# Kernel tuning notes

Measured on AMD Instinct MI355X. Metric: run time of the kernel, lower is better.

## Reference

```python
import jax, jax.numpy as jnp
from jax import lax
import numpy as np

B = 8192
NUM_CTX = 300; NUM_STN = 300; NUM_GPE = 20; NUM_GPI = 2; NUM_OUT = 20
FF_DIM = 20; FF_STEPS = 20; STN_ITERS = 50
ETA_GPE = 1.0; ETA_STN = 1.0 / 3.0; ETA_GPI = 0.1
A1 = 1.0; A2 = 1.0; THETAD1 = 0.0; THETAD2 = 0.0
UNITS = (64, 128, 64)

_SPECS = [("vf0", UNITS[0], NUM_CTX), ("vf1", UNITS[1], UNITS[0]), ("vf2", UNITS[2], UNITS[1]), ("vf3", 1, UNITS[2]),
          ("jd1", FF_DIM, NUM_CTX), ("jd2", FF_DIM, NUM_CTX), ("kd1", FF_DIM, NUM_CTX), ("kd2", FF_DIM, NUM_CTX),
          ("sg", NUM_GPE, NUM_STN), ("gs", NUM_STN, NUM_GPE), ("glat", NUM_GPE, NUM_GPE), ("slat", NUM_STN, NUM_STN),
          ("d1gpi", NUM_GPI, FF_DIM), ("stngpi", NUM_GPI, NUM_STN),
          ("ih", 4 * NUM_OUT, NUM_GPI), ("hh", 4 * NUM_OUT, NUM_OUT)]


def _lin_init(k, out_d, in_d):
    kw, kb = jax.random.split(k)
    bound = 1.0 / np.sqrt(in_d)
    w = jax.random.uniform(kw, (out_d, in_d), minval=-bound, maxval=bound, dtype=jnp.float32)
    b = jax.random.uniform(kb, (out_d,), minval=-bound, maxval=bound, dtype=jnp.float32)
    return w, b


def setup_inputs() -> dict:
    key = jax.random.key(0)
    ks = iter(jax.random.split(key, 40))
    inp = {}
    inp["stimulus"] = jax.random.normal(next(ks), (B, NUM_CTX), dtype=jnp.float32)
    inp["deltavf"] = jax.random.normal(next(ks), (B, 1), dtype=jnp.float32)
    inp["hx0"] = jax.random.uniform(next(ks), (B, NUM_OUT), dtype=jnp.float32)
    inp["cx0"] = jax.random.uniform(next(ks), (B, NUM_OUT), dtype=jnp.float32)
    for name, o, i in _SPECS:
        w, b = _lin_init(next(ks), o, i)
        inp["w_" + name] = w
        inp["b_" + name] = b
    return inp


def _lin(x, w, b):
    return x @ w.T + b


def _lstm_cell(x, h, c, w_ih, b_ih, w_hh, b_hh):
    gates = _lin(x, w_ih, b_ih) + _lin(h, w_hh, b_hh)
    i, f, g, o = jnp.split(gates, 4, axis=-1)  # torch LSTMCell gate order
    c_new = jax.nn.sigmoid(f) * c + jax.nn.sigmoid(i) * jnp.tanh(g)
    h_new = jax.nn.sigmoid(o) * jnp.tanh(c_new)
    return h_new, c_new


def reference(stimulus, deltavf, hx0, cx0,
              w_vf0, b_vf0, w_vf1, b_vf1, w_vf2, b_vf2, w_vf3, b_vf3,
              w_jd1, b_jd1, w_jd2, b_jd2, w_kd1, b_kd1, w_kd2, b_kd2,
              w_sg, b_sg, w_gs, b_gs, w_glat, b_glat, w_slat, b_slat,
              w_d1gpi, b_d1gpi, w_stngpi, b_stngpi,
              w_ih, b_ih, w_hh, b_hh):
    bsz = stimulus.shape[0]
    # value function head
    h = jax.nn.relu(_lin(stimulus, w_vf0, b_vf0))
    h = jax.nn.relu(_lin(h, w_vf1, b_vf1))
    h = jax.nn.relu(_lin(h, w_vf2, b_vf2))
    vt = jnp.tanh(_lin(h, w_vf3, b_vf3))  # [B, 1]

    lamd1 = jax.nn.sigmoid(A1 * (deltavf - THETAD1))  # [B, 1]
    lamd2 = jax.nn.sigmoid(A2 * (deltavf - THETAD2))  # [B, 1]

    # loop-invariant striatal drives (computed every iter in torch, same value)
    J_D1 = _lin(stimulus, w_jd1, b_jd1)
    J_D2 = _lin(stimulus, w_jd2, b_jd2)
    K_D1 = _lin(stimulus, w_kd1, b_kd1)
    K_D2 = _lin(stimulus, w_kd2, b_kd2)

    def ff_step(carry, _):
        v1, v2 = carry
        v1 = jax.nn.sigmoid(lamd1 * (J_D1 * (1.0 - v1) + (1.0 - K_D1) * v1))
        v2 = jax.nn.sigmoid(lamd2 * (J_D2 * (1.0 - v2) + (1.0 - K_D2) * v2))
        return (v1, v2), None

    z_ff = jnp.zeros((bsz, FF_DIM), dtype=stimulus.dtype)
    (V_D1, V_D2), _ = lax.scan(ff_step, (z_ff, z_ff), None, length=FF_STEPS)

    V_GPi_DP = _lin(V_D1, w_d1gpi, b_d1gpi)  # [B, num_gpi]

    def stn_step(carry, _):
        xgpe, xstn, vstn, vgpi, hx, cx = carry
        xgpe = xgpe + ETA_GPE * (-xgpe + _lin(vstn, w_sg, b_sg) + _lin(xgpe, w_glat, b_glat) - V_D2)
        xstn = xstn + ETA_STN * (-xstn + _lin(xgpe, w_gs, b_gs) + _lin(vstn, w_slat, b_slat))
        vstn = jnp.tanh(lamd2 * xstn)
        V_GPi_IP = lamd2 * _lin(vstn, w_stngpi, b_stngpi)
        vgpi = vgpi + ETA_GPI * (-vgpi - V_GPi_DP + 2.0 * V_GPi_IP)
        hx, cx = _lstm_cell(-vgpi, hx, cx, w_ih, b_ih, w_hh, b_hh)
        return (xgpe, xstn, vstn, vgpi, hx, cx), None

    carry0 = (jnp.zeros((bsz, NUM_GPE), dtype=stimulus.dtype),
              jnp.zeros((bsz, NUM_STN), dtype=stimulus.dtype),
              jnp.zeros((bsz, NUM_STN), dtype=stimulus.dtype),  # tanh(lamd2*0) = 0
              jnp.zeros((bsz, NUM_GPI), dtype=stimulus.dtype),
              hx0, cx0)
    carry, _ = lax.scan(stn_step, carry0, None, length=STN_ITERS)
    hx = carry[4]
    return hx, vt
```

## Files before the change

### kernel.cpp

```cpp
#include <hip/hip_runtime.h>


typedef _Float16 f16_t;
typedef _Float16 f16x8 __attribute__((ext_vector_type(8)));
typedef _Float16 f16x4 __attribute__((ext_vector_type(4)));
typedef float floatx4 __attribute__((ext_vector_type(4)));
typedef float floatx2 __attribute__((ext_vector_type(2)));

#define BTOT 8192
#define BM   32
#define NTHR 512
#define NBLK 256
#define VSTR 328
#define XST  32

struct Params {
  const float *stimulus, *deltavf, *hx0, *cx0;
  const float *w_vf0, *b_vf0, *w_vf1, *b_vf1, *w_vf2, *b_vf2, *w_vf3, *b_vf3;
  const float *w_jd1, *b_jd1, *w_jd2, *b_jd2, *w_kd1, *b_kd1, *w_kd2, *b_kd2;
  const float *w_sg, *b_sg, *w_gs, *b_gs, *w_glat, *b_glat, *w_slat, *b_slat;
  const float *w_d1gpi, *b_d1gpi, *w_stngpi, *b_stngpi;
  const float *w_ih, *b_ih, *w_hh, *b_hh;
  float* out;
};

struct __align__(16) Smem {
  f16_t vstn[BM * VSTR];
  f16_t xgpe[2][BM * XST];
  f16_t hxf[BM * XST];
  f16_t wB2[21 * 512];
  f16_t wsp[10 * 512];
  f16_t whh[5 * 512];
  union { float h1f[BM * 128]; float scr[3200]; float gates[BM * 80]; } u;
  float h0f[BM * 64];
  float V_D2f[BM * 20];
  float lstmc[20][12];
  float bsumS[304];
  float bsg[20];
  float DPs[BM * 2], vgpis[BM * 2], lamS[BM];
};

__device__ __forceinline__ float rcp_f(float x) { return __builtin_amdgcn_rcpf(x); }
__device__ __forceinline__ float sigm_fast(float x) { return rcp_f(1.f + __expf(-x)); }
__device__ __forceinline__ float tanh_fast(float x) { return 1.f - 2.f * rcp_f(1.f + __expf(2.f * x)); }

__device__ __forceinline__ f16x8 ldfrag(const float* row, int k0, int kmax, bool valid) {
  float4 z = make_float4(0.f, 0.f, 0.f, 0.f);
  int nv = valid ? (kmax - k0) : 0;
  float4 f0 = (nv >= 4) ? *(const float4*)(row + k0) : z;
  float4 f1 = (nv >= 8) ? *(const float4*)(row + k0 + 4) : z;
  f16x8 r;
  r[0] = (f16_t)f0.x; r[1] = (f16_t)f0.y; r[2] = (f16_t)f0.z; r[3] = (f16_t)f0.w;
  r[4] = (f16_t)f1.x; r[5] = (f16_t)f1.y; r[6] = (f16_t)f1.z; r[7] = (f16_t)f1.w;
  return r;
}

__global__ __launch_bounds__(NTHR, 2) void bg_main(Params P) {
  __shared__ Smem S;
  const int tid  = threadIdx.x;
  const int lane = tid & 63;
  const int wv   = tid >> 6;
  const int q    = lane >> 4;
  const int cl   = lane & 15;
  const int row0 = blockIdx.x * BM;
  const floatx4 zf = {0.f, 0.f, 0.f, 0.f};

  if (tid < BM) S.lamS[tid] = sigm_fast(P.deltavf[row0 + tid]);
  for (int i = tid; i < BM * 2; i += NTHR) S.vgpis[i] = 0.f;
  for (int i = tid; i < 2 * BM * XST; i += NTHR) ((f16_t*)S.xgpe)[i] = (f16_t)0.f;
  for (int i = tid; i < BM * XST; i += NTHR) {
    int m = i >> 5, j = i & 31;
    S.hxf[i] = (j < 20) ? (f16_t)P.hx0[row0 * 20 + m * 20 + j] : (f16_t)0.f;
  }
  for (int i = tid; i < BM * VSTR; i += NTHR) S.vstn[i] = (f16_t)0.f;
  for (int i = tid; i < 21 * 512; i += NTHR) {
    int t = i >> 9, l = (i >> 3) & 63, jj = i & 7;
    int c2 = l & 15, k = ((l >> 4) << 3) + jj;
    float v = 0.f;
    if (t < 19) { int n = t * 16 + c2; if (n < 300 && k < 20) v = P.w_gs[n * 20 + k]; }
    else        { int g = (t - 19) * 16 + c2; if (g < 20 && k < 20) v = P.w_glat[g * 20 + k]; }
    S.wB2[i] = (f16_t)v;
  }
  for (int i = tid; i < 10 * 512; i += NTHR) {
    int c = i >> 9, l = (i >> 3) & 63, jj = i & 7;
    int p = l & 15, k = c * 32 + ((l >> 4) << 3) + jj;
    float v = (p < 2 && k < 300) ? P.w_stngpi[p * 300 + k] : 0.f;
    S.wsp[i] = (f16_t)v;
  }
  for (int i = tid; i < 5 * 512; i += NTHR) {
    int t = i >> 9, l = (i >> 3) & 63, jj = i & 7;
    int c2 = l & 15, k = ((l >> 4) << 3) + jj;
    int orig = (c2 & 3) * 20 + 4 * t + (c2 >> 2);
    S.whh[i] = (f16_t)((k < 20) ? P.w_hh[orig * 20 + k] : 0.f);
  }
  for (int i = tid; i < 240; i += NTHR) {
    int j = i / 12, c = i - j * 12;
    float v;
    if (c < 4)      v = P.b_ih[c * 20 + j] + P.b_hh[c * 20 + j];
    else if (c < 8) v = P.w_ih[((c - 4) * 20 + j) * 2 + 0];
    else            v = P.w_ih[((c - 8) * 20 + j) * 2 + 1];
    S.lstmc[j][c] = v;
  }
  for (int i = tid; i < 304; i += NTHR) S.bsumS[i] = (i < 300) ? (P.b_slat[i] + P.b_gs[i]) : 0.f;
  for (int i = tid; i < 20; i += NTHR)  S.bsg[i] = P.b_sg[i] + P.b_glat[i];

  {
    int o = tid & 63, mb = (tid >> 6) * 4;
    const float4* wr = (const float4*)(P.w_vf0 + o * 300);
    float bias = P.b_vf0[o], a[4];
#pragma unroll
    for (int u = 0; u < 4; ++u) a[u] = bias;
    for (int kq = 0; kq < 75; ++kq) {
      float4 w = wr[kq];
#pragma unroll
      for (int u = 0; u < 4; ++u) {
        float4 v = *(const float4*)(P.stimulus + (size_t)(row0 + mb + u) * 300 + kq * 4);
        a[u] = fmaf(v.x, w.x, a[u]); a[u] = fmaf(v.y, w.y, a[u]);
        a[u] = fmaf(v.z, w.z, a[u]); a[u] = fmaf(v.w, w.w, a[u]);
      }
    }
#pragma unroll
    for (int u = 0; u < 4; ++u) S.h0f[(mb + u) * 64 + o] = fmaxf(a[u], 0.f);
  }
  __syncthreads();
  {
    int o = tid & 127, mb = (tid >> 7) * 8;
    const float* wr = P.w_vf1 + o * 64;
    float bias = P.b_vf1[o], a[8];
#pragma unroll
    for (int u = 0; u < 8; ++u) a[u] = bias;
    for (int k = 0; k < 64; ++k) {
      float w = wr[k];
#pragma unroll
      for (int u = 0; u < 8; ++u) a[u] = fmaf(S.h0f[(mb + u) * 64 + k], w, a[u]);
    }
#pragma unroll
    for (int u = 0; u < 8; ++u) S.u.h1f[(mb + u) * 128 + o] = fmaxf(a[u], 0.f);
  }
  __syncthreads();
  {
    int o = tid & 63, mb = (tid >> 6) * 4;
    const float* wr = P.w_vf2 + o * 128;
    float bias = P.b_vf2[o], a[4];
#pragma unroll
    for (int u = 0; u < 4; ++u) a[u] = bias;
    for (int k = 0; k < 128; ++k) {
      float w = wr[k];
#pragma unroll
      for (int u = 0; u < 4; ++u) a[u] = fmaf(S.u.h1f[(mb + u) * 128 + k], w, a[u]);
    }
#pragma unroll
    for (int u = 0; u < 4; ++u) S.h0f[(mb + u) * 64 + o] = fmaxf(a[u], 0.f);
  }
  __syncthreads();
  {
    int oid = tid & 127, mb = (tid >> 7) * 8;
    if (oid < 80) {
      int which = oid / 20, o = oid - which * 20;
      const float *wp, *bp;
      if (which == 0)      { wp = P.w_jd1; bp = P.b_jd1; }
      else if (which == 1) { wp = P.w_jd2; bp = P.b_jd2; }
      else if (which == 2) { wp = P.w_kd1; bp = P.b_kd1; }
      else                 { wp = P.w_kd2; bp = P.b_kd2; }
      float bias = bp[o], a[8];
#pragma unroll
      for (int u = 0; u < 8; ++u) a[u] = bias;
      for (int kq = 0; kq < 75; ++kq) {
        float4 w = *(const float4*)(wp + o * 300 + kq * 4);
#pragma unroll
        for (int u = 0; u < 8; ++u) {
          float4 v = *(const float4*)(P.stimulus + (size_t)(row0 + mb + u) * 300 + kq * 4);
          a[u] = fmaf(v.x, w.x, a[u]); a[u] = fmaf(v.y, w.y, a[u]);
          a[u] = fmaf(v.z, w.z, a[u]); a[u] = fmaf(v.w, w.w, a[u]);
        }
      }
#pragma unroll
      for (int u = 0; u < 8; ++u) S.u.scr[which * 640 + (mb + u) * 20 + o] = a[u];
    }
    if (tid < BM) {
      float a = P.b_vf3[0];
      for (int k = 0; k < 64; ++k) a = fmaf(S.h0f[tid * 64 + k], P.w_vf3[k], a);
      P.out[(size_t)BTOT * 20 + row0 + tid] = tanh_fast(a);
    }
  }
  __syncthreads();
  for (int i = tid; i < BM * 20; i += NTHR) {
    int m = i / 20;
    float j1 = S.u.scr[i],        j2 = S.u.scr[640 + i];
    float k1 = S.u.scr[1280 + i], k2 = S.u.scr[1920 + i];
    float L = S.lamS[m], v1 = 0.f, v2 = 0.f;
    for (int s = 0; s < 20; ++s) {
      v1 = sigm_fast(L * (j1 * (1.f - v1) + (1.f - k1) * v1));
      v2 = sigm_fast(L * (j2 * (1.f - v2) + (1.f - k2) * v2));
    }
    S.u.scr[2560 + i] = v1;
    S.V_D2f[i] = v2;
  }
  __syncthreads();
  if (tid < BM * 2) {
    int m = tid >> 1, p2 = tid & 1;
    float a = P.b_d1gpi[p2];
    for (int o = 0; o < 20; ++o) a = fmaf(S.u.scr[2560 + m * 20 + o], P.w_d1gpi[p2 * 20 + o], a);
    S.DPs[tid] = a;
  }
  __syncthreads();

  f16x8 Ws[3][10];
#pragma unroll
  for (int j = 0; j < 3; ++j) {
    int t = wv + 8 * j;
    if (t < 19) {
      int n = t * 16 + cl;
#pragma unroll
      for (int c = 0; c < 10; ++c)
        Ws[j][c] = ldfrag(P.w_slat + (size_t)(n < 300 ? n : 0) * 300, c * 32 + q * 8, 300, n < 300);
    } else if (t < 21) {
      int g = (t - 19) * 16 + cl;
#pragma unroll
      for (int c = 0; c < 10; ++c)
        Ws[j][c] = ldfrag(P.w_sg + (size_t)(g < 20 ? g : 0) * 300, c * 32 + q * 8, 300, g < 20);
    } else {
      f16x8 z;
#pragma unroll
      for (int e = 0; e < 8; ++e) z[e] = (f16_t)0.f;
#pragma unroll
      for (int c = 0; c < 10; ++c) Ws[j][c] = z;
    }
  }
  const float lam0 = S.lamS[cl], lam1 = S.lamS[cl + 16];
  const float bstn0 = P.b_stngpi[0], bstn1 = P.b_stngpi[1];
  const int e0 = tid,        m0 = e0 / 20, j0 = e0 - m0 * 20;
  const int e1 = tid + NTHR, m1 = e1 / 20, j1 = e1 - m1 * 20;
  const bool hase1 = (tid < BM * 20 - NTHR);
  float cxr0 = P.cx0[row0 * 20 + e0], hxr0 = P.hx0[row0 * 20 + e0];
  float cxr1 = hase1 ? P.cx0[row0 * 20 + e1] : 0.f;
  float hxr1 = hase1 ? P.hx0[row0 * 20 + e1] : 0.f;
  const bool isSgW = (wv == 3 || wv == 4);

  floatx4 acc[3][2];
#pragma unroll
  for (int j = 0; j < 3; ++j) { acc[j][0] = zf; acc[j][1] = zf; }

  for (int g = 0; g <= 50; ++g) {
    const bool run = (g < 50), ran = (g > 0);
    const int po = g & 1, pn = po ^ 1;

    if (run) {
      if (isSgW) { acc[2][0] = zf; acc[2][1] = zf; }
      __builtin_amdgcn_s_setprio(1);
#pragma unroll
      for (int c = 0; c < 10; ++c) {
        f16x8 b0 = *(const f16x8*)&S.vstn[cl * VSTR + c * 32 + q * 8];
        f16x8 b1 = *(const f16x8*)&S.vstn[(16 + cl) * VSTR + c * 32 + q * 8];
#pragma unroll
        for (int j = 0; j < 3; ++j) {
          if (wv + 8 * j < 21) {
            acc[j][0] = __builtin_amdgcn_mfma_f32_16x16x32_f16(Ws[j][c], b0, acc[j][0], 0, 0, 0);
            acc[j][1] = __builtin_amdgcn_mfma_f32_16x16x32_f16(Ws[j][c], b1, acc[j][1], 0, 0, 0);
          }
        }
      }
      __builtin_amdgcn_s_setprio(0);
      if (isSgW) {
        f16x8 Wg = *(const f16x8*)&S.wB2[(wv + 16) * 512 + lane * 8];
        f16x8 g0 = *(const f16x8*)&S.xgpe[po][cl * XST + q * 8];
        f16x8 g1 = *(const f16x8*)&S.xgpe[po][(16 + cl) * XST + q * 8];
        acc[2][0] = __builtin_amdgcn_mfma_f32_16x16x32_f16(Wg, g0, acc[2][0], 0, 0, 0);
        acc[2][1] = __builtin_amdgcn_mfma_f32_16x16x32_f16(Wg, g1, acc[2][1], 0, 0, 0);
        int g0i = (wv - 3) * 16 + q * 4;
        if (g0i < 20) {
          floatx4 bg4 = *(const floatx4*)&S.bsg[g0i];
#pragma unroll
          for (int mf = 0; mf < 2; ++mf) {
            int batch = cl + 16 * mf;
            floatx4 vd4 = *(const floatx4*)&S.V_D2f[batch * 20 + g0i];
            f16x4 pk;
#pragma unroll
            for (int r = 0; r < 4; ++r) pk[r] = (f16_t)(acc[2][mf][r] + bg4[r] - vd4[r]);
            *(f16x4*)&S.xgpe[pn][batch * XST + g0i] = pk;
          }
        }
      }
    }
    if (ran && wv == 5) {
      floatx4 ip0 = zf, ip1 = zf;
#pragma unroll
      for (int c = 0; c < 10; ++c) {
        f16x8 Wp = *(const f16x8*)&S.wsp[c * 512 + lane * 8];
        f16x8 b0 = *(const f16x8*)&S.vstn[cl * VSTR + c * 32 + q * 8];
        f16x8 b1 = *(const f16x8*)&S.vstn[(16 + cl) * VSTR + c * 32 + q * 8];
        ip0 = __builtin_amdgcn_mfma_f32_16x16x32_f16(Wp, b0, ip0, 0, 0, 0);
        ip1 = __builtin_amdgcn_mfma_f32_16x16x32_f16(Wp, b1, ip1, 0, 0, 0);
      }
      if (q == 0) {
#pragma unroll
        for (int mf = 0; mf < 2; ++mf) {
          int batch = cl + 16 * mf;
          float lm = mf ? lam1 : lam0;
          floatx2 vg = *(const floatx2*)&S.vgpis[batch * 2];
          floatx2 dp = *(const floatx2*)&S.DPs[batch * 2];
          float ipa = lm * ((mf ? ip1[0] : ip0[0]) + bstn0);
          float ipb = lm * ((mf ? ip1[1] : ip0[1]) + bstn1);
          vg[0] = vg[0] + 0.1f * (-vg[0] - dp[0] + 2.f * ipa);
          vg[1] = vg[1] + 0.1f * (-vg[1] - dp[1] + 2.f * ipb);
          *(floatx2*)&S.vgpis[batch * 2] = vg;
        }
      }
    }
    if (ran && (wv == 6 || wv == 7)) {
      int tb = (wv == 6) ? 0 : 3;
      int tc = (wv == 6) ? 3 : 2;
      for (int tt = 0; tt < tc; ++tt) {
        int t = tb + tt;
        f16x8 Wh = *(const f16x8*)&S.whh[t * 512 + lane * 8];
        f16x8 h0 = *(const f16x8*)&S.hxf[cl * XST + q * 8];
        f16x8 h1 = *(const f16x8*)&S.hxf[(16 + cl) * XST + q * 8];
        floatx4 gA = __builtin_amdgcn_mfma_f32_16x16x32_f16(Wh, h0, zf, 0, 0, 0);
        floatx4 gB = __builtin_amdgcn_mfma_f32_16x16x32_f16(Wh, h1, zf, 0, 0, 0);
        int gb = t * 16 + q * 4;
        *(floatx4*)&S.u.gates[cl * 80 + gb] = gA;
        *(floatx4*)&S.u.gates[(cl + 16) * 80 + gb] = gB;
      }
    }
    __syncthreads();

    if (run) {
      f16x8 x0 = *(const f16x8*)&S.xgpe[pn][cl * XST + q * 8];
      f16x8 x1 = *(const f16x8*)&S.xgpe[pn][(16 + cl) * XST + q * 8];
#pragma unroll
      for (int j = 0; j < 3; ++j) {
        int t = wv + 8 * j;
        if (t < 19) {
          f16x8 Wg = *(const f16x8*)&S.wB2[t * 512 + lane * 8];
          acc[j][0] = __builtin_amdgcn_mfma_f32_16x16x32_f16(Wg, x0, acc[j][0], 0, 0, 0);
          acc[j][1] = __builtin_amdgcn_mfma_f32_16x16x32_f16(Wg, x1, acc[j][1], 0, 0, 0);
        }
      }
#pragma unroll
      for (int j = 0; j < 3; ++j) {
        int t = wv + 8 * j;
        if (t < 19) {
          int n0 = t * 16 + q * 4;
          if (!(t == 18 && q == 3)) {
            floatx4 bs4 = *(const floatx4*)&S.bsumS[n0];
#pragma unroll
            for (int mf = 0; mf < 2; ++mf) {
              float lm = mf ? lam1 : lam0;
              f16x4 pk;
#pragma unroll
              for (int r = 0; r < 4; ++r) {
                float tmp = acc[j][mf][r] + bs4[r];
                float xn  = tmp * (1.0f / 3.0f);
                acc[j][mf][r] = tmp * (2.0f / 3.0f);
                pk[r] = (f16_t)tanh_fast(lm * xn);
              }
              *(f16x4*)&S.vstn[(cl + 16 * mf) * VSTR + n0] = pk;
            }
          }
        }
      }
    }
    if (ran) {
      {
        floatx4 g4 = *(const floatx4*)&S.u.gates[m0 * 80 + j0 * 4];
        floatx4 cb = *(const floatx4*)&S.lstmc[j0][0];
        floatx4 w0 = *(const floatx4*)&S.lstmc[j0][4];
        floatx4 w1 = *(const floatx4*)&S.lstmc[j0][8];
        floatx2 vg = *(const floatx2*)&S.vgpis[m0 * 2];
        float gi = g4[0] + cb[0] - w0[0] * vg[0] - w1[0] * vg[1];
        float gf = g4[1] + cb[1] - w0[1] * vg[0] - w1[1] * vg[1];
        float gg = g4[2] + cb[2] - w0[2] * vg[0] - w1[2] * vg[1];
        float go = g4[3] + cb[3] - w0[3] * vg[0] - w1[3] * vg[1];
        float cn = sigm_fast(gf) * cxr0 + sigm_fast(gi) * tanh_fast(gg);
        cxr0 = cn;
        hxr0 = sigm_fast(go) * tanh_fast(cn);
        S.hxf[m0 * XST + j0] = (f16_t)hxr0;
      }
      if (hase1) {
        floatx4 g4 = *(const floatx4*)&S.u.gates[m1 * 80 + j1 * 4];
        floatx4 cb = *(const floatx4*)&S.lstmc[j1][0];
        floatx4 w0 = *(const floatx4*)&S.lstmc[j1][4];
        floatx4 w1 = *(const floatx4*)&S.lstmc[j1][8];
        floatx2 vg = *(const floatx2*)&S.vgpis[m1 * 2];
        float gi = g4[0] + cb[0] - w0[0] * vg[0] - w1[0] * vg[1];
        float gf = g4[1] + cb[1] - w0[1] * vg[0] - w1[1] * vg[1];
        float gg = g4[2] + cb[2] - w0[2] * vg[0] - w1[2] * vg[1];
        float go = g4[3] + cb[3] - w0[3] * vg[0] - w1[3] * vg[1];
        float cn = sigm_fast(gf) * cxr1 + sigm_fast(gi) * tanh_fast(gg);
        cxr1 = cn;
        hxr1 = sigm_fast(go) * tanh_fast(cn);
        S.hxf[m1 * XST + j1] = (f16_t)hxr1;
      }
    }
    __syncthreads();
  }

  P.out[(size_t)row0 * 20 + e0] = hxr0;
  if (hase1) P.out[(size_t)row0 * 20 + e1] = hxr1;
}

extern "C" void kernel_launch(void* const* d_in, const int* in_sizes, int n_in,
                              void* d_out, int out_size, void* d_ws, size_t ws_size,
                              hipStream_t stream) {
  (void)in_sizes; (void)n_in; (void)out_size; (void)d_ws; (void)ws_size;
  Params P;
  P.stimulus = (const float*)d_in[0];
  P.deltavf  = (const float*)d_in[1];
  P.hx0 = (const float*)d_in[2];
  P.cx0 = (const float*)d_in[3];
  P.w_vf0 = (const float*)d_in[4];  P.b_vf0 = (const float*)d_in[5];
  P.w_vf1 = (const float*)d_in[6];  P.b_vf1 = (const float*)d_in[7];
  P.w_vf2 = (const float*)d_in[8];  P.b_vf2 = (const float*)d_in[9];
  P.w_vf3 = (const float*)d_in[10]; P.b_vf3 = (const float*)d_in[11];
  P.w_jd1 = (const float*)d_in[12]; P.b_jd1 = (const float*)d_in[13];
  P.w_jd2 = (const float*)d_in[14]; P.b_jd2 = (const float*)d_in[15];
  P.w_kd1 = (const float*)d_in[16]; P.b_kd1 = (const float*)d_in[17];
  P.w_kd2 = (const float*)d_in[18]; P.b_kd2 = (const float*)d_in[19];
  P.w_sg  = (const float*)d_in[20]; P.b_sg  = (const float*)d_in[21];
  P.w_gs  = (const float*)d_in[22]; P.b_gs  = (const float*)d_in[23];
  P.w_glat= (const float*)d_in[24]; P.b_glat= (const float*)d_in[25];
  P.w_slat= (const float*)d_in[26]; P.b_slat= (const float*)d_in[27];
  P.w_d1gpi  = (const float*)d_in[28]; P.b_d1gpi  = (const float*)d_in[29];
  P.w_stngpi = (const float*)d_in[30]; P.b_stngpi = (const float*)d_in[31];
  P.w_ih = (const float*)d_in[32]; P.b_ih = (const float*)d_in[33];
  P.w_hh = (const float*)d_in[34]; P.b_hh = (const float*)d_in[35];
  P.out  = (float*)d_out;
  bg_main<<<NBLK, NTHR, 0, stream>>>(P);
}
```

Measured before the change: 396.5 us.

## Fold GPe update into STN recurrence via precomposed weights and per-batch bias

Substitutes the GPe update into the STN update. Because ETA_GPE is 1, the new xgpe is a linear function of vstn and the old xgpe. The kernel therefore precomputes W_slat + W_gs·W_sg, W_gs·W_glat, and a per-batch bias W_gs·(b_sg − V_D2) + bsum, so each step's xstn can be computed from the previous vstn and xgpe in the same phase, before the first barrier. vstn is double-buffered to allow this, and the old second-phase STN MFMA and tanh block is removed. This shortens the serial dependency chain per iteration. The cost is extra setup work, more LDS (a roughly 39KB bias table and a second vstn buffer), and extra fp16 rounding error from the precomposed weights.

```diff
diff --git a/kernel.cpp b/kernel.cpp
--- a/kernel.cpp
+++ b/kernel.cpp
@@ -25,13 +25,17 @@
 };
 
 struct __align__(16) Smem {
-  f16_t vstn[BM * VSTR];
+  f16_t vstn[2][BM * VSTR];
   f16_t xgpe[2][BM * XST];
   f16_t hxf[BM * XST];
   f16_t wB2[21 * 512];
   f16_t wsp[10 * 512];
   f16_t whh[5 * 512];
-  union { float h1f[BM * 128]; float scr[3200]; float gates[BM * 80]; } u;
+  union {
+    float h1f[BM * 128];
+    float scr[3200];
+    struct { float gates[BM * 80]; float biasB[32 * 304]; } L;
+  } u;
   float h0f[BM * 64];
   float V_D2f[BM * 20];
   float lstmc[20][12];
@@ -55,6 +59,32 @@
   return r;
 }
 
+__device__ __forceinline__ f16x8 ldfrag_eff(const float* slatrow, const float* gsr,
+                                            const float* sgbase, int k0, bool valid) {
+  float4 z = make_float4(0.f, 0.f, 0.f, 0.f);
+  int nv = valid ? (300 - k0) : 0;
+  float4 f0 = (nv >= 4) ? *(const float4*)(slatrow + k0) : z;
+  float4 f1 = (nv >= 8) ? *(const float4*)(slatrow + k0 + 4) : z;
+  float a0 = f0.x, a1 = f0.y, a2 = f0.z, a3 = f0.w;
+  float a4 = f1.x, a5 = f1.y, a6 = f1.z, a7 = f1.w;
+  if (nv > 0) {
+    for (int p = 0; p < 20; ++p) {
+      float g = gsr[p];
+      const float* sr = sgbase + p * 300 + k0;
+      float4 s0 = (nv >= 4) ? *(const float4*)(sr) : z;
+      float4 s1 = (nv >= 8) ? *(const float4*)(sr + 4) : z;
+      a0 = fmaf(g, s0.x, a0); a1 = fmaf(g, s0.y, a1);
+      a2 = fmaf(g, s0.z, a2); a3 = fmaf(g, s0.w, a3);
+      a4 = fmaf(g, s1.x, a4); a5 = fmaf(g, s1.y, a5);
+      a6 = fmaf(g, s1.z, a6); a7 = fmaf(g, s1.w, a7);
+    }
+  }
+  f16x8 r;
+  r[0] = (f16_t)a0; r[1] = (f16_t)a1; r[2] = (f16_t)a2; r[3] = (f16_t)a3;
+  r[4] = (f16_t)a4; r[5] = (f16_t)a5; r[6] = (f16_t)a6; r[7] = (f16_t)a7;
+  return r;
+}
+
 __global__ __launch_bounds__(NTHR, 2) void bg_main(Params P) {
   __shared__ Smem S;
   const int tid  = threadIdx.x;
@@ -72,13 +102,23 @@
     int m = i >> 5, j = i & 31;
     S.hxf[i] = (j < 20) ? (f16_t)P.hx0[row0 * 20 + m * 20 + j] : (f16_t)0.f;
   }
-  for (int i = tid; i < BM * VSTR; i += NTHR) S.vstn[i] = (f16_t)0.f;
+  for (int i = tid; i < 2 * BM * VSTR; i += NTHR) ((f16_t*)S.vstn)[i] = (f16_t)0.f;
   for (int i = tid; i < 21 * 512; i += NTHR) {
     int t = i >> 9, l = (i >> 3) & 63, jj = i & 7;
     int c2 = l & 15, k = ((l >> 4) << 3) + jj;
     float v = 0.f;
-    if (t < 19) { int n = t * 16 + c2; if (n < 300 && k < 20) v = P.w_gs[n * 20 + k]; }
-    else        { int g = (t - 19) * 16 + c2; if (g < 20 && k < 20) v = P.w_glat[g * 20 + k]; }
+    if (t < 19) {
+      int n = t * 16 + c2;
+      if (n < 300 && k < 20) {
+        const float* gr = P.w_gs + n * 20;
+        float a = 0.f;
+        for (int p = 0; p < 20; ++p) a = fmaf(gr[p], P.w_glat[p * 20 + k], a);
+        v = a;
+      }
+    } else {
+      int g = (t - 19) * 16 + c2;
+      if (g < 20 && k < 20) v = P.w_glat[g * 20 + k];
+    }
     S.wB2[i] = (f16_t)v;
   }
   for (int i = tid; i < 10 * 512; i += NTHR) {
@@ -204,6 +244,17 @@
     S.DPs[tid] = a;
   }
   __syncthreads();
+  for (int i = tid; i < 32 * 304; i += NTHR) {
+    int b = i / 304, n = i - b * 304;
+    float v = 0.f;
+    if (n < 300) {
+      const float* gr = P.w_gs + n * 20;
+      float a = S.bsumS[n];
+      for (int p = 0; p < 20; ++p) a = fmaf(gr[p], S.bsg[p] - S.V_D2f[b * 20 + p], a);
+      v = a;
+    }
+    S.u.L.biasB[i] = v;
+  }
 
   f16x8 Ws[3][10];
 #pragma unroll
@@ -211,9 +262,15 @@
     int t = wv + 8 * j;
     if (t < 19) {
       int n = t * 16 + cl;
+      bool valid = (n < 300);
+      const float* srow = P.w_slat + (size_t)(valid ? n : 0) * 300;
+      const float* grow = P.w_gs + (size_t)(valid ? n : 0) * 20;
+      float gsr[20];
+#pragma unroll
+      for (int p = 0; p < 20; ++p) gsr[p] = grow[p];
 #pragma unroll
       for (int c = 0; c < 10; ++c)
-        Ws[j][c] = ldfrag(P.w_slat + (size_t)(n < 300 ? n : 0) * 300, c * 32 + q * 8, 300, n < 300);
+        Ws[j][c] = ldfrag_eff(srow, gsr, P.w_sg, c * 32 + q * 8, valid);
     } else if (t < 21) {
       int g = (t - 19) * 16 + cl;
 #pragma unroll
@@ -227,6 +284,8 @@
       for (int c = 0; c < 10; ++c) Ws[j][c] = z;
     }
   }
+  __syncthreads();
+
   const float lam0 = S.lamS[cl], lam1 = S.lamS[cl + 16];
   const float bstn0 = P.b_stngpi[0], bstn1 = P.b_stngpi[1];
   const int e0 = tid,        m0 = e0 / 20, j0 = e0 - m0 * 20;
@@ -243,15 +302,15 @@
 
   for (int g = 0; g <= 50; ++g) {
     const bool run = (g < 50), ran = (g > 0);
-    const int po = g & 1, pn = po ^ 1;
+    const int wr = g & 1, rd = wr ^ 1;
 
     if (run) {
       if (isSgW) { acc[2][0] = zf; acc[2][1] = zf; }
       __builtin_amdgcn_s_setprio(1);
 #pragma unroll
       for (int c = 0; c < 10; ++c) {
-        f16x8 b0 = *(const f16x8*)&S.vstn[cl * VSTR + c * 32 + q * 8];
-        f16x8 b1 = *(const f16x8*)&S.vstn[(16 + cl) * VSTR + c * 32 + q * 8];
+        f16x8 b0 = *(const f16x8*)&S.vstn[rd][cl * VSTR + c * 32 + q * 8];
+        f16x8 b1 = *(const f16x8*)&S.vstn[rd][(16 + cl) * VSTR + c * 32 + q * 8];
 #pragma unroll
         for (int j = 0; j < 3; ++j) {
           if (wv + 8 * j < 21) {
@@ -260,24 +319,59 @@
           }
         }
       }
+      {
+        f16x8 xg0 = *(const f16x8*)&S.xgpe[rd][cl * XST + q * 8];
+        f16x8 xg1 = *(const f16x8*)&S.xgpe[rd][(16 + cl) * XST + q * 8];
+#pragma unroll
+        for (int j = 0; j < 3; ++j) {
+          int t = wv + 8 * j;
+          if (t < 19) {
+            f16x8 Wg = *(const f16x8*)&S.wB2[t * 512 + lane * 8];
+            acc[j][0] = __builtin_amdgcn_mfma_f32_16x16x32_f16(Wg, xg0, acc[j][0], 0, 0, 0);
+            acc[j][1] = __builtin_amdgcn_mfma_f32_16x16x32_f16(Wg, xg1, acc[j][1], 0, 0, 0);
+          }
+        }
+        if (isSgW) {
+          f16x8 Wg = *(const f16x8*)&S.wB2[(wv + 16) * 512 + lane * 8];
+          acc[2][0] = __builtin_amdgcn_mfma_f32_16x16x32_f16(Wg, xg0, acc[2][0], 0, 0, 0);
+          acc[2][1] = __builtin_amdgcn_mfma_f32_16x16x32_f16(Wg, xg1, acc[2][1], 0, 0, 0);
+          int g0i = (wv - 3) * 16 + q * 4;
+          if (g0i < 20) {
+            floatx4 bg4 = *(const floatx4*)&S.bsg[g0i];
+#pragma unroll
+            for (int mf = 0; mf < 2; ++mf) {
+              int batch = cl + 16 * mf;
+              floatx4 vd4 = *(const floatx4*)&S.V_D2f[batch * 20 + g0i];
+              f16x4 pk;
+#pragma unroll
+              for (int r = 0; r < 4; ++r) pk[r] = (f16_t)(acc[2][mf][r] + bg4[r] - vd4[r]);
+              *(f16x4*)&S.xgpe[wr][batch * XST + g0i] = pk;
+            }
+          }
+        }
+      }
       __builtin_amdgcn_s_setprio(0);
-      if (isSgW) {
-        f16x8 Wg = *(const f16x8*)&S.wB2[(wv + 16) * 512 + lane * 8];
-        f16x8 g0 = *(const f16x8*)&S.xgpe[po][cl * XST + q * 8];
-        f16x8 g1 = *(const f16x8*)&S.xgpe[po][(16 + cl) * XST + q * 8];
-        acc[2][0] = __builtin_amdgcn_mfma_f32_16x16x32_f16(Wg, g0, acc[2][0], 0, 0, 0);
-        acc[2][1] = __builtin_amdgcn_mfma_f32_16x16x32_f16(Wg, g1, acc[2][1], 0, 0, 0);
-        int g0i = (wv - 3) * 16 + q * 4;
-        if (g0i < 20) {
-          floatx4 bg4 = *(const floatx4*)&S.bsg[g0i];
-#pragma unroll
-          for (int mf = 0; mf < 2; ++mf) {
-            int batch = cl + 16 * mf;
-            floatx4 vd4 = *(const floatx4*)&S.V_D2f[batch * 20 + g0i];
-            f16x4 pk;
-#pragma unroll
-            for (int r = 0; r < 4; ++r) pk[r] = (f16_t)(acc[2][mf][r] + bg4[r] - vd4[r]);
-            *(f16x4*)&S.xgpe[pn][batch * XST + g0i] = pk;
+#pragma unroll
+      for (int j = 0; j < 3; ++j) {
+        int t = wv + 8 * j;
+        if (t < 19) {
+          int n0 = t * 16 + q * 4;
+          if (!(t == 18 && q == 3)) {
+#pragma unroll
+            for (int mf = 0; mf < 2; ++mf) {
+              int batch = cl + 16 * mf;
+              float lm = mf ? lam1 : lam0;
+              floatx4 bb = *(const floatx4*)&S.u.L.biasB[batch * 304 + n0];
+              f16x4 pk;
+#pragma unroll
+              for (int r = 0; r < 4; ++r) {
+                float tmp = acc[j][mf][r] + bb[r];
+                float xn  = tmp * (1.0f / 3.0f);
+                acc[j][mf][r] = tmp * (2.0f / 3.0f);
+                pk[r] = (f16_t)tanh_fast(lm * xn);
+              }
+              *(f16x4*)&S.vstn[wr][batch * VSTR + n0] = pk;
+            }
           }
         }
       }
@@ -287,8 +381,8 @@
 #pragma unroll
       for (int c = 0; c < 10; ++c) {
         f16x8 Wp = *(const f16x8*)&S.wsp[c * 512 + lane * 8];
-        f16x8 b0 = *(const f16x8*)&S.vstn[cl * VSTR + c * 32 + q * 8];
-        f16x8 b1 = *(const f16x8*)&S.vstn[(16 + cl) * VSTR + c * 32 + q * 8];
+        f16x8 b0 = *(const f16x8*)&S.vstn[rd][cl * VSTR + c * 32 + q * 8];
+        f16x8 b1 = *(const f16x8*)&S.vstn[rd][(16 + cl) * VSTR + c * 32 + q * 8];
         ip0 = __builtin_amdgcn_mfma_f32_16x16x32_f16(Wp, b0, ip0, 0, 0, 0);
         ip1 = __builtin_amdgcn_mfma_f32_16x16x32_f16(Wp, b1, ip1, 0, 0, 0);
       }
@@ -318,51 +412,15 @@
         floatx4 gA = __builtin_amdgcn_mfma_f32_16x16x32_f16(Wh, h0, zf, 0, 0, 0);
         floatx4 gB = __builtin_amdgcn_mfma_f32_16x16x32_f16(Wh, h1, zf, 0, 0, 0);
         int gb = t * 16 + q * 4;
-        *(floatx4*)&S.u.gates[cl * 80 + gb] = gA;
-        *(floatx4*)&S.u.gates[(cl + 16) * 80 + gb] = gB;
+        *(floatx4*)&S.u.L.gates[cl * 80 + gb] = gA;
+        *(floatx4*)&S.u.L.gates[(cl + 16) * 80 + gb] = gB;
       }
     }
     __syncthreads();
 
-    if (run) {
-      f16x8 x0 = *(const f16x8*)&S.xgpe[pn][cl * XST + q * 8];
-      f16x8 x1 = *(const f16x8*)&S.xgpe[pn][(16 + cl) * XST + q * 8];
-#pragma unroll
-      for (int j = 0; j < 3; ++j) {
-        int t = wv + 8 * j;
-        if (t < 19) {
-          f16x8 Wg = *(const f16x8*)&S.wB2[t * 512 + lane * 8];
-          acc[j][0] = __builtin_amdgcn_mfma_f32_16x16x32_f16(Wg, x0, acc[j][0], 0, 0, 0);
-          acc[j][1] = __builtin_amdgcn_mfma_f32_16x16x32_f16(Wg, x1, acc[j][1], 0, 0, 0);
-        }
-      }
-#pragma unroll
-      for (int j = 0; j < 3; ++j) {
-        int t = wv + 8 * j;
-        if (t < 19) {
-          int n0 = t * 16 + q * 4;
-          if (!(t == 18 && q == 3)) {
-            floatx4 bs4 = *(const floatx4*)&S.bsumS[n0];
-#pragma unroll
-            for (int mf = 0; mf < 2; ++mf) {
-              float lm = mf ? lam1 : lam0;
-              f16x4 pk;
-#pragma unroll
-              for (int r = 0; r < 4; ++r) {
-                float tmp = acc[j][mf][r] + bs4[r];
-                float xn  = tmp * (1.0f / 3.0f);
-                acc[j][mf][r] = tmp * (2.0f / 3.0f);
-                pk[r] = (f16_t)tanh_fast(lm * xn);
-              }
-              *(f16x4*)&S.vstn[(cl + 16 * mf) * VSTR + n0] = pk;
-            }
-          }
-        }
-      }
-    }
     if (ran) {
       {
-        floatx4 g4 = *(const floatx4*)&S.u.gates[m0 * 80 + j0 * 4];
+        floatx4 g4 = *(const floatx4*)&S.u.L.gates[m0 * 80 + j0 * 4];
         floatx4 cb = *(const floatx4*)&S.lstmc[j0][0];
         floatx4 w0 = *(const floatx4*)&S.lstmc[j0][4];
         floatx4 w1 = *(const floatx4*)&S.lstmc[j0][8];
@@ -377,7 +435,7 @@
         S.hxf[m0 * XST + j0] = (f16_t)hxr0;
       }
       if (hase1) {
-        floatx4 g4 = *(const floatx4*)&S.u.gates[m1 * 80 + j1 * 4];
+        floatx4 g4 = *(const floatx4*)&S.u.L.gates[m1 * 80 + j1 * 4];
         floatx4 cb = *(const floatx4*)&S.lstmc[j1][0];
         floatx4 w0 = *(const floatx4*)&S.lstmc[j1][4];
         floatx4 w1 = *(const floatx4*)&S.lstmc[j1][8];
```

Result: slower. 1.255 ms (+216.5%).
